# Kernel optimization log

Measured on AMD Instinct MI355X. Metric: run time of the kernel, lower is better.

The kernel has to match this reference:

```python
import jax, jax.numpy as jnp
import numpy as np

IN_DIM, H1, H2, H3, LATENT = 1024, 1024, 512, 256, 256
D, K, BETA = 32, 2048, 0.25
B = 16384


def _leaky(x):
    return jax.nn.leaky_relu(x, negative_slope=0.01)


def setup_inputs() -> dict:
    key = jax.random.key(0)
    ks = jax.random.split(key, 18)
    def lin(k, fan_in, fan_out):
        kw, kb = jax.random.split(k)
        s = 1.0 / np.sqrt(fan_in)
        W = jax.random.uniform(kw, (fan_in, fan_out), jnp.float32, -s, s)
        b = jax.random.uniform(kb, (fan_out,), jnp.float32, -s, s)
        return W, b
    We1, be1 = lin(ks[0], IN_DIM, H1)
    We2, be2 = lin(ks[1], H1, H2)
    We3, be3 = lin(ks[2], H2, H3)
    We4, be4 = lin(ks[3], H3, LATENT)
    Wd1, bd1 = lin(ks[4], LATENT, H3)
    Wd2, bd2 = lin(ks[5], H3, H2)
    Wd3, bd3 = lin(ks[6], H2, H1)
    Wd4, bd4 = lin(ks[7], H1, IN_DIM)
    E = jax.random.uniform(ks[8], (K, D), jnp.float32, -1.0 / K, 1.0 / K)  # codebook
    x = jax.random.uniform(ks[9], (B, IN_DIM), jnp.float32)
    return {"x": x, "We1": We1, "be1": be1, "We2": We2, "be2": be2,
            "We3": We3, "be3": be3, "We4": We4, "be4": be4, "E": E,
            "Wd1": Wd1, "bd1": bd1, "Wd2": Wd2, "bd2": bd2,
            "Wd3": Wd3, "bd3": bd3, "Wd4": Wd4, "bd4": bd4}


def reference(x, We1, be1, We2, be2, We3, be3, We4, be4, E,
              Wd1, bd1, Wd2, bd2, Wd3, bd3, Wd4, bd4):
    # encoder MLP
    h = _leaky(x @ We1 + be1)
    h = _leaky(h @ We2 + be2)
    h = _leaky(h @ We3 + be3)
    z = h @ We4 + be4                      # [B, LATENT]
    # vector quantizer
    zr = z.reshape(-1, D)                  # [N, D], N = B*LATENT/D
    dist = (jnp.sum(zr * zr, axis=1, keepdims=True)
            + jnp.sum(E * E, axis=1)
            - 2.0 * zr @ E.T)              # [N, K]
    idx = jnp.argmin(dist, axis=1)         # [N]
    # one-hot @ E == direct gather of nearest codebook rows
    q = E[idx].reshape(z.shape)            # [B, LATENT]
    commit = jnp.mean(jnp.sum(jnp.square(jax.lax.stop_gradient(q) - z), axis=1))
    embed = jnp.mean(jnp.sum(jnp.square(q - jax.lax.stop_gradient(z)), axis=1))
    vq_loss = BETA * commit + embed
    e = z + jax.lax.stop_gradient(q - z)   # straight-through
    # decoder MLP
    h = _leaky(e @ Wd1 + bd1)
    h = _leaky(h @ Wd2 + bd2)
    h = _leaky(h @ Wd3 + bd3)
    recon = jax.nn.sigmoid(h @ Wd4 + bd4)
    recon_loss = jnp.mean(jnp.sum(jnp.square(recon - x), axis=-1))
    loss = recon_loss + vq_loss
    return z, e, recon, loss, recon_loss, vq_loss
```

## Files before the change

kernel.cpp:

```cpp
#include <hip/hip_runtime.h>
#include <stdint.h>

typedef __attribute__((ext_vector_type(8))) _Float16 half8;
typedef __attribute__((ext_vector_type(4))) _Float16 half4;
typedef __attribute__((ext_vector_type(4))) float f32x4;

__device__ __forceinline__ void gload_lds16(const void* g, void* l) {
  __builtin_amdgcn_global_load_lds(
      (const __attribute__((address_space(1))) void*)g,
      (__attribute__((address_space(3))) void*)l, 16, 0, 0);
}

template <int EPI, int BM, int BN>
__global__ __launch_bounds__(256, ((BM + BN) >= 256 ? 2 : ((BM + BN) == 192 ? 3 : 4)))
void gemm_bt(
    const _Float16* __restrict__ A, const _Float16* __restrict__ Bt,
    const float* __restrict__ bias, _Float16* __restrict__ Ch,
    float* __restrict__ Cf, int M, int N, int Kd,
    const _Float16* __restrict__ Xref, float* __restrict__ lossAcc) {
  constexpr int WM = BM / 2, WN = BN / 2;
  constexpr int MF = WM / 16, NF = WN / 16;
  constexpr int CA = BM / 32, CB = BN / 32;
  constexpr int CHUNKS = CA + CB;
  constexpr int STAGE = (BM + BN) * 64;
  __shared__ __align__(16) _Float16 smem[2 * STAGE];
  float* red = (float*)smem + 64 * BN;

  const int tid = threadIdx.x;
  const int lane = tid & 63;
  const int wav = tid >> 6;
  const int nx = gridDim.x;
  const int nwg = nx * (int)gridDim.y;
  int bid = (int)blockIdx.y * nx + (int)blockIdx.x;
  bid = (bid & 7) * (nwg >> 3) + (bid >> 3);
  const int shift = 31 - __clz(nx);
  const int m0 = (bid >> shift) * BM;
  const int n0 = (bid & (nx - 1)) * BN;
  const int wm = (wav >> 1) * WM;
  const int wn = (wav & 1) * WN;
  const int l15 = lane & 15;
  const int quad = lane >> 4;

  f32x4 acc[MF][NF];
#pragma unroll
  for (int i = 0; i < MF; i++)
#pragma unroll
    for (int j = 0; j < NF; j++) acc[i][j] = (f32x4){0.f, 0.f, 0.f, 0.f};

  auto issue = [&](int kt, int b) {
    _Float16* As = smem + b * STAGE;
    _Float16* Bs = As + BM * 64;
#pragma unroll
    for (int j = 0; j < CA; j++) {
      const int ci = j * 256 + tid;
      const int row = ci >> 3;
      const int kc = ((ci & 7) ^ (row & 7)) << 3;
      gload_lds16(A + (size_t)(m0 + row) * Kd + kt + kc, &As[ci * 8]);
    }
#pragma unroll
    for (int j = 0; j < CB; j++) {
      const int ci = j * 256 + tid;
      const int row = ci >> 3;
      const int kc = ((ci & 7) ^ (row & 7)) << 3;
      gload_lds16(Bt + (size_t)(n0 + row) * Kd + kt + kc, &Bs[ci * 8]);
    }
  };

  int buf = 0;
  issue(0, 0);
  for (int kt = 0; kt < Kd; kt += 64) {
    if (kt + 64 < Kd) {
      issue(kt + 64, buf ^ 1);
      asm volatile("s_waitcnt vmcnt(%0)" ::"i"(CHUNKS) : "memory");
    } else {
      asm volatile("s_waitcnt vmcnt(0)" ::: "memory");
    }
    asm volatile("s_barrier" ::: "memory");

    const _Float16* As = smem + buf * STAGE;
    const _Float16* Bs = As + BM * 64;
#pragma unroll
    for (int s = 0; s < 2; s++) {
      half8 af[MF], bq[NF];
#pragma unroll
      for (int i = 0; i < MF; i++) {
        const int ra = wm + i * 16 + l15;
        const int ca = (s * 4 + quad) ^ (ra & 7);
        af[i] = *(const half8*)&As[ra * 64 + ca * 8];
      }
#pragma unroll
      for (int i = 0; i < NF; i++) {
        const int rb = wn + i * 16 + l15;
        const int cb = (s * 4 + quad) ^ (rb & 7);
        bq[i] = *(const half8*)&Bs[rb * 64 + cb * 8];
      }
#pragma unroll
      for (int mi = 0; mi < MF; mi++)
#pragma unroll
        for (int ni = 0; ni < NF; ni++)
          acc[mi][ni] = __builtin_amdgcn_mfma_f32_16x16x32_f16(af[mi], bq[ni],
                                                               acc[mi][ni], 0, 0, 0);
    }
    asm volatile("s_barrier" ::: "memory");
    buf ^= 1;
  }

  float lsum = 0.f;
  float* eb = (float*)smem;
  constexpr int DIV = BN / 4;
#pragma unroll
  for (int p = 0; p < BM / 64; p++) {
    __syncthreads();
    if ((wm >> 6) == p) {
#pragma unroll
      for (int mi = 0; mi < MF; mi++)
#pragma unroll
        for (int ni = 0; ni < NF; ni++)
#pragma unroll
          for (int r = 0; r < 4; r++) {
            const int rl = (wm & 63) + mi * 16 + quad * 4 + r;
            const int cl = wn + ni * 16 + l15;
            eb[rl * BN + cl] = acc[mi][ni][r];
          }
    }
    __syncthreads();
#pragma unroll
    for (int j = 0; j < BN / 16; j++) {
      const int c = j * 256 + tid;
      const int rl = c / DIV;
      const int cl = (c % DIV) * 4;
      const f32x4 v = *(const f32x4*)&eb[rl * BN + cl];
      const int gcol = n0 + cl;
      const f32x4 bv = *(const f32x4*)&bias[gcol];
      const size_t o = (size_t)(m0 + p * 64 + rl) * N + gcol;
      if (EPI == 0) {
        half4 h;
#pragma unroll
        for (int q = 0; q < 4; q++) {
          float t = v[q] + bv[q];
          t = t > 0.f ? t : 0.01f * t;
          h[q] = (_Float16)t;
        }
        *(half4*)&Ch[o] = h;
      } else if (EPI == 1) {
        f32x4 t;
        half4 h;
#pragma unroll
        for (int q = 0; q < 4; q++) {
          t[q] = v[q] + bv[q];
          h[q] = (_Float16)t[q];
        }
        *(f32x4*)&Cf[o] = t;
        *(half4*)&Ch[o] = h;
      } else {
        const half4 xr = *(const half4*)&Xref[o];
        f32x4 sv;
#pragma unroll
        for (int q = 0; q < 4; q++) {
          const float s = 1.f / (1.f + __expf(-(v[q] + bv[q])));
          sv[q] = s;
          const float d = s - (float)xr[q];
          lsum += d * d;
        }
        *(f32x4*)&Cf[o] = sv;
      }
    }
  }
  if (EPI == 2) {
    __syncthreads();
    red[tid] = lsum;
    __syncthreads();
    for (int s = 128; s > 0; s >>= 1) {
      if (tid < s) red[tid] += red[tid + s];
      __syncthreads();
    }
    if (tid == 0) atomicAdd(lossAcc, red[0]);
  }
}

__global__ __launch_bounds__(256, 4) void vq_argmin(
    const _Float16* __restrict__ zh, const _Float16* __restrict__ Ehf,
    const float* __restrict__ E, const float* __restrict__ ek2,
    float* __restrict__ e_out, _Float16* __restrict__ eh_out,
    float* __restrict__ vq_acc) {
  __shared__ __align__(16) _Float16 Es[512 * 32];
  __shared__ float ek2s[512];
  __shared__ float z2s[128];
  __shared__ int idxs[128];
  __shared__ float vred[256];

  const int tid = threadIdx.x;
  const int lane = tid & 63;
  const int wav = tid >> 6;
  const int l15 = lane & 15;
  const int quad = lane >> 4;
  const int rbase = blockIdx.x * 128 + wav * 32;
  constexpr unsigned KEYMASK = 0xFFFFF800u;

  half8 zf[2];
  float z2p[2];
#pragma unroll
  for (int m = 0; m < 2; m++) {
    zf[m] = *(const half8*)(zh + ((size_t)(rbase + m * 16 + l15)) * 32 + quad * 8);
    float s = 0.f;
#pragma unroll
    for (int j = 0; j < 8; j++) {
      float v = (float)zf[m][j];
      s += v * v;
    }
    s += __shfl_xor(s, 16);
    s += __shfl_xor(s, 32);
    z2p[m] = s;
  }
  if (quad == 0) {
#pragma unroll
    for (int m = 0; m < 2; m++) z2s[wav * 32 + m * 16 + l15] = z2p[m];
  }

  float key[2][4];
#pragma unroll
  for (int m = 0; m < 2; m++)
#pragma unroll
    for (int r = 0; r < 4; r++) key[m][r] = 1e30f;

  for (int cb = 0; cb < 2048; cb += 512) {
    __syncthreads();
#pragma unroll
    for (int j = 0; j < 8; j++) {
      const int u = j * 256 + tid;
      gload_lds16(Ehf + (size_t)cb * 32 + u * 8, &Es[u * 8]);
    }
    if (tid < 128) gload_lds16(&ek2[cb + tid * 4], &ek2s[tid * 4]);
    __syncthreads();

    int idxv = cb + l15;
    for (int c16 = 0; c16 < 32; c16++) {
      const half8 ef = *(const half8*)&Es[(c16 * 64 + lane) * 8];
      const float e2 = ek2s[c16 * 16 + l15];
      const f32x4 cinit = (f32x4){e2, e2, e2, e2};
      f32x4 d0 = __builtin_amdgcn_mfma_f32_16x16x32_f16(zf[0], ef, cinit, 0, 0, 0);
      f32x4 d1 = __builtin_amdgcn_mfma_f32_16x16x32_f16(zf[1], ef, cinit, 0, 0, 0);
#pragma unroll
      for (int r = 0; r < 4; r++) {
        key[0][r] = fminf(key[0][r],
                          __uint_as_float((__float_as_uint(d0[r]) & KEYMASK) | idxv));
        key[1][r] = fminf(key[1][r],
                          __uint_as_float((__float_as_uint(d1[r]) & KEYMASK) | idxv));
      }
      idxv += 16;
    }
  }

#pragma unroll
  for (int off = 1; off < 16; off <<= 1)
#pragma unroll
    for (int m = 0; m < 2; m++)
#pragma unroll
      for (int r = 0; r < 4; r++)
        key[m][r] = fminf(key[m][r], __shfl_xor(key[m][r], off));

  float vpart = 0.f;
  if (l15 == 0) {
#pragma unroll
    for (int m = 0; m < 2; m++)
#pragma unroll
      for (int r = 0; r < 4; r++) {
        const unsigned kb = __float_as_uint(key[m][r]);
        const int rl = wav * 32 + m * 16 + quad * 4 + r;
        idxs[rl] = (int)(kb & 0x7FFu);
        vpart += z2s[rl] + __uint_as_float(kb & KEYMASK);
      }
  }
  vred[tid] = vpart;
  __syncthreads();
  for (int s = 128; s > 0; s >>= 1) {
    if (tid < s) vred[tid] += vred[tid + s];
    __syncthreads();
  }
  if (tid == 0) atomicAdd(vq_acc, vred[0]);

#pragma unroll
  for (int it = 0; it < 2; it++) {
    const int slot = it * 256 + tid;
    const int rowb = slot >> 2, part = slot & 3;
    const int idx = idxs[rowb];
    const size_t orow = ((size_t)blockIdx.x * 128 + rowb) * 32 + part * 8;
    const f32x4 ea = *(const f32x4*)(E + (size_t)idx * 32 + part * 8);
    const f32x4 ebv = *(const f32x4*)(E + (size_t)idx * 32 + part * 8 + 4);
    *(f32x4*)(e_out + orow) = ea;
    *(f32x4*)(e_out + orow + 4) = ebv;
    half8 ehv;
#pragma unroll
    for (int j = 0; j < 4; j++) {
      ehv[j] = (_Float16)ea[j];
      ehv[j + 4] = (_Float16)ebv[j];
    }
    *(half8*)(eh_out + orow) = ehv;
  }
}

struct PrepArgs {
  const float* W[8];
  _Float16* Wt[8];
  int Kw[8], Nw[8];
  int base[9];
  const float* x;
  _Float16* xh;
  const float* E;
  _Float16* Ehf;
  float* ek2;
};

__global__ __launch_bounds__(256) void prep_k(PrepArgs a) {
  __shared__ float t[32][33];
  const int b = blockIdx.x;
  const int tid = threadIdx.x;
  if (b < 8192) {
    const size_t i = (size_t)b * 256 + tid;
    const f32x4 va = *(const f32x4*)(a.x + i * 8);
    const f32x4 vb = *(const f32x4*)(a.x + i * 8 + 4);
    half8 h;
#pragma unroll
    for (int j = 0; j < 4; j++) {
      h[j] = (_Float16)va[j];
      h[j + 4] = (_Float16)vb[j];
    }
    *(half8*)(a.xh + i * 8) = h;
    return;
  }
  if (b < 8192 + 3456) {
    int l = b - 8192;
    int w = 0;
    while (l >= a.base[w + 1]) w++;
    l -= a.base[w];
    const float* W = a.W[w];
    _Float16* Wt = a.Wt[w];
    const int K = a.Kw[w], N = a.Nw[w];
    const int nb = N >> 5;
    const int bx = (l % nb) * 32, by = (l / nb) * 32;
    const int tx = tid & 31, ty = tid >> 5;
#pragma unroll
    for (int i = 0; i < 32; i += 8)
      t[ty + i][tx] = W[(size_t)(by + ty + i) * N + bx + tx];
    __syncthreads();
#pragma unroll
    for (int i = 0; i < 32; i += 8)
      Wt[(size_t)(bx + ty + i) * K + by + tx] = (_Float16)t[tx][ty + i];
    return;
  }
  const int c = (b - 8192 - 3456) * 256 + tid;
  float s = 0.f;
#pragma unroll
  for (int k = 0; k < 32; k++) {
    const float v = a.E[(size_t)c * 32 + k];
    s += v * v;
    a.Ehf[(size_t)((c >> 4) * 64 + (k >> 3) * 16 + (c & 15)) * 8 + (k & 7)] =
        (_Float16)(-2.f * v);
  }
  a.ek2[c] = s;
}

__global__ void finalize_k(const float* __restrict__ scal, float* __restrict__ out) {
  const float vq = 1.25f * (scal[0] / 16384.f);
  const float rl = scal[1] / 16384.f;
  out[0] = rl + vq;
  out[1] = rl;
  out[2] = vq;
}

extern "C" void kernel_launch(void* const* d_in, const int* in_sizes, int n_in,
                              void* d_out, int out_size, void* d_ws, size_t ws_size,
                              hipStream_t stream) {
  const float* x = (const float*)d_in[0];
  const float* be1 = (const float*)d_in[2];
  const float* be2 = (const float*)d_in[4];
  const float* be3 = (const float*)d_in[6];
  const float* be4 = (const float*)d_in[8];
  const float* E = (const float*)d_in[9];
  const float* bd1 = (const float*)d_in[11];
  const float* bd2 = (const float*)d_in[13];
  const float* bd3 = (const float*)d_in[15];
  const float* bd4 = (const float*)d_in[17];

  float* out = (float*)d_out;
  char* ws = (char*)d_ws;

  size_t off = 0;
  auto alloc = [&](size_t bytes) {
    size_t r = off;
    off += (bytes + 255) & ~(size_t)255;
    return r;
  };
  const size_t oXH = alloc((size_t)16384 * 1024 * 2);
  const size_t oWT1 = alloc((size_t)1024 * 1024 * 2);
  const size_t oWT2 = alloc((size_t)512 * 1024 * 2);
  const size_t oWT3 = alloc((size_t)256 * 512 * 2);
  const size_t oWT4 = alloc((size_t)256 * 256 * 2);
  const size_t oWD1 = alloc((size_t)256 * 256 * 2);
  const size_t oWD2 = alloc((size_t)512 * 256 * 2);
  const size_t oWD3 = alloc((size_t)1024 * 512 * 2);
  const size_t oWD4 = alloc((size_t)1024 * 1024 * 2);
  const size_t oEHF = alloc((size_t)2048 * 32 * 2);
  const size_t oEK2 = alloc((size_t)2048 * 4);
  const size_t oSC = alloc(256);
  const size_t oZH = alloc((size_t)16384 * 256 * 2);
  const size_t oQH = alloc((size_t)16384 * 256 * 2);
  const size_t oH1 = alloc((size_t)16384 * 1024 * 2);
  const size_t oH2 = alloc((size_t)16384 * 512 * 2);
  const size_t oH3 = alloc((size_t)16384 * 256 * 2);

  _Float16* xh = (_Float16*)(ws + oXH);
  _Float16* WT1 = (_Float16*)(ws + oWT1);
  _Float16* WT2 = (_Float16*)(ws + oWT2);
  _Float16* WT3 = (_Float16*)(ws + oWT3);
  _Float16* WT4 = (_Float16*)(ws + oWT4);
  _Float16* WD1 = (_Float16*)(ws + oWD1);
  _Float16* WD2 = (_Float16*)(ws + oWD2);
  _Float16* WD3 = (_Float16*)(ws + oWD3);
  _Float16* WD4 = (_Float16*)(ws + oWD4);
  _Float16* Ehf = (_Float16*)(ws + oEHF);
  float* ek2 = (float*)(ws + oEK2);
  float* scal = (float*)(ws + oSC);
  _Float16* zhw = (_Float16*)(ws + oZH);
  _Float16* qh = (_Float16*)(ws + oQH);
  _Float16* h1 = (_Float16*)(ws + oH1);
  _Float16* h2 = (_Float16*)(ws + oH2);
  _Float16* h3 = (_Float16*)(ws + oH3);

  float* zout = out;
  float* eout = out + (size_t)16384 * 256;
  float* rout = out + (size_t)16384 * 256 * 2;
  float* sout = rout + (size_t)16384 * 1024;

  hipMemsetAsync(ws + oSC, 0, 8, stream);

  PrepArgs pa;
  pa.W[0] = (const float*)d_in[1];  pa.Wt[0] = WT1; pa.Kw[0] = 1024; pa.Nw[0] = 1024;
  pa.W[1] = (const float*)d_in[3];  pa.Wt[1] = WT2; pa.Kw[1] = 1024; pa.Nw[1] = 512;
  pa.W[2] = (const float*)d_in[5];  pa.Wt[2] = WT3; pa.Kw[2] = 512;  pa.Nw[2] = 256;
  pa.W[3] = (const float*)d_in[7];  pa.Wt[3] = WT4; pa.Kw[3] = 256;  pa.Nw[3] = 256;
  pa.W[4] = (const float*)d_in[10]; pa.Wt[4] = WD1; pa.Kw[4] = 256;  pa.Nw[4] = 256;
  pa.W[5] = (const float*)d_in[12]; pa.Wt[5] = WD2; pa.Kw[5] = 256;  pa.Nw[5] = 512;
  pa.W[6] = (const float*)d_in[14]; pa.Wt[6] = WD3; pa.Kw[6] = 512;  pa.Nw[6] = 1024;
  pa.W[7] = (const float*)d_in[16]; pa.Wt[7] = WD4; pa.Kw[7] = 1024; pa.Nw[7] = 1024;
  int acc = 0;
  for (int w = 0; w < 8; w++) {
    pa.base[w] = acc;
    acc += (pa.Kw[w] >> 5) * (pa.Nw[w] >> 5);
  }
  pa.base[8] = acc;
  pa.x = x; pa.xh = xh; pa.E = E; pa.Ehf = Ehf; pa.ek2 = ek2;

  dim3 blk(256);
  prep_k<<<8192 + 3456 + 8, blk, 0, stream>>>(pa);

  gemm_bt<0, 128, 128><<<dim3(8, 128), blk, 0, stream>>>(
      xh, WT1, be1, h1, nullptr, 16384, 1024, 1024, nullptr, nullptr);
  gemm_bt<0, 128, 128><<<dim3(4, 128), blk, 0, stream>>>(
      h1, WT2, be2, h2, nullptr, 16384, 512, 1024, nullptr, nullptr);
  gemm_bt<0, 64, 64><<<dim3(4, 256), blk, 0, stream>>>(
      h2, WT3, be3, h3, nullptr, 16384, 256, 512, nullptr, nullptr);
  gemm_bt<1, 64, 64><<<dim3(4, 256), blk, 0, stream>>>(
      h3, WT4, be4, zhw, zout, 16384, 256, 256, nullptr, nullptr);
  vq_argmin<<<1024, blk, 0, stream>>>(zhw, Ehf, E, ek2, eout, qh, &scal[0]);
  gemm_bt<0, 64, 64><<<dim3(4, 256), blk, 0, stream>>>(
      qh, WD1, bd1, h3, nullptr, 16384, 256, 256, nullptr, nullptr);
  gemm_bt<0, 128, 128><<<dim3(4, 128), blk, 0, stream>>>(
      h3, WD2, bd2, h2, nullptr, 16384, 512, 256, nullptr, nullptr);
  gemm_bt<0, 128, 128><<<dim3(8, 128), blk, 0, stream>>>(
      h2, WD3, bd3, h1, nullptr, 16384, 1024, 512, nullptr, nullptr);
  gemm_bt<2, 128, 128><<<dim3(8, 128), blk, 0, stream>>>(
      h1, WD4, bd4, nullptr, rout, 16384, 1024, 1024, xh, &scal[1]);
  finalize_k<<<1, 1, 0, stream>>>(scal, sout);
}
```

Before: 397.7 us.

## Add 256x256-tile 8-wave pipelined GEMM for the three largest layers

Adds a new GEMM kernel with 256x256 output tiles, 8 waves and 128KB of dynamic LDS. It double-buffers K tiles, splits each tile into four sub-blocks whose loads are interleaved with MFMA phases, and raises wave priority around the MFMAs. It also remaps workgroup IDs in an XCD-aware order. The kernel replaces the 128x128 kernel for the encoder's first layer and the last two decoder layers, aiming for more data reuse per load and better overlap of loads with MFMA work. The cost is fewer, larger workgroups (256 per launch) and heavy LDS and register use, which may limit occupancy and wave balance across CUs.

```diff
diff --git a/kernel.cpp b/kernel.cpp
--- a/kernel.cpp
+++ b/kernel.cpp
@@ -9,6 +9,211 @@
   __builtin_amdgcn_global_load_lds(
       (const __attribute__((address_space(1))) void*)g,
       (__attribute__((address_space(3))) void*)l, 16, 0, 0);
+}
+
+#define GBAR asm volatile("s_barrier" ::: "memory")
+#define LGKM0                                            \
+  asm volatile("s_waitcnt lgkmcnt(0)" ::: "memory");     \
+  __builtin_amdgcn_sched_barrier(0)
+
+#define MMA_Q(QM, QN)                                                        \
+  __builtin_amdgcn_s_setprio(1);                                             \
+  _Pragma("unroll") for (int s = 0; s < 2; s++)                              \
+  _Pragma("unroll") for (int i = 0; i < 4; i++)                              \
+  _Pragma("unroll") for (int j = 0; j < 2; j++)                              \
+      acc[(QM) * 4 + i][(QN) * 2 + j] = __builtin_amdgcn_mfma_f32_16x16x32_f16( \
+          af[i][s], bq[j][s], acc[(QM) * 4 + i][(QN) * 2 + j], 0, 0, 0);     \
+  __builtin_amdgcn_s_setprio(0);
+
+template <int EPI>
+__global__ __launch_bounds__(512, 2) void gemm8p(
+    const _Float16* __restrict__ A, const _Float16* __restrict__ Bt,
+    const float* __restrict__ bias, _Float16* __restrict__ Ch,
+    float* __restrict__ Cf, int M, int N, int Kd,
+    const _Float16* __restrict__ Xref, float* __restrict__ lossAcc) {
+  extern __shared__ __align__(16) char dyn[];
+
+  const int tid = threadIdx.x;
+  const int lane = tid & 63;
+  const int wav = tid >> 6;
+  const int wr = wav >> 2;
+  const int wc = wav & 3;
+  const int l15 = lane & 15;
+  const int quad = lane >> 4;
+
+  const int nx = gridDim.x;
+  const int nwg = nx * (int)gridDim.y;
+  int bid = (int)blockIdx.y * nx + (int)blockIdx.x;
+  bid = (bid & 7) * (nwg >> 3) + (bid >> 3);
+  const int shift = 31 - __clz(nx);
+  const int m0 = (bid >> shift) * 256;
+  const int n0 = (bid & (nx - 1)) * 256;
+
+  f32x4 acc[8][4];
+#pragma unroll
+  for (int i = 0; i < 8; i++)
+#pragma unroll
+    for (int j = 0; j < 4; j++) acc[i][j] = (f32x4){0.f, 0.f, 0.f, 0.f};
+
+  auto stageA = [&](int kt, int slot, int RB) {
+    const int row = RB + (tid >> 3);
+    const int ch = tid & 7;
+    const int gm = m0 + ((row >> 6) & 1) * 128 + (row >> 7) * 64 + (row & 63);
+    const int kc = (ch ^ (row & 7)) << 3;
+    gload_lds16(A + (size_t)gm * Kd + kt + kc,
+                dyn + slot * 65536 + row * 128 + ch * 16);
+  };
+  auto stageB = [&](int kt, int slot, int RB) {
+    const int row = RB + (tid >> 3);
+    const int ch = tid & 7;
+    const int gn = n0 + ((row >> 5) & 3) * 64 + (row >> 7) * 32 + (row & 31);
+    const int kc = (ch ^ (row & 7)) << 3;
+    gload_lds16(Bt + (size_t)gn * Kd + kt + kc,
+                dyn + slot * 65536 + 32768 + row * 128 + ch * 16);
+  };
+
+  half8 af[4][2], bq[2][2];
+  auto dsA = [&](const _Float16* As, int qm) {
+#pragma unroll
+    for (int i = 0; i < 4; i++) {
+      const int ra = qm * 128 + wr * 64 + i * 16 + l15;
+#pragma unroll
+      for (int s = 0; s < 2; s++)
+        af[i][s] = *(const half8*)&As[ra * 64 + (((s * 4 + quad) ^ (ra & 7)) << 3)];
+    }
+  };
+  auto dsB = [&](const _Float16* Bs, int qn) {
+#pragma unroll
+    for (int j = 0; j < 2; j++) {
+      const int rb = qn * 128 + wc * 32 + j * 16 + l15;
+#pragma unroll
+      for (int s = 0; s < 2; s++)
+        bq[j][s] = *(const half8*)&Bs[rb * 64 + (((s * 4 + quad) ^ (rb & 7)) << 3)];
+    }
+  };
+
+  const int NT = Kd >> 6;
+
+  stageA(0, 0, 0);
+  stageA(0, 0, 64);
+  stageB(0, 0, 128);
+  stageB(0, 0, 192);
+  stageA(0, 0, 128);
+  stageA(0, 0, 192);
+  stageB(0, 0, 0);
+  stageB(0, 0, 64);
+  stageA(64, 1, 0);
+  stageA(64, 1, 64);
+  stageB(64, 1, 128);
+  stageB(64, 1, 192);
+  asm volatile("s_waitcnt vmcnt(4)" ::: "memory");
+  GBAR;
+
+  for (int t = 0; t < NT; ++t) {
+    const int slot = t & 1;
+    const int nsl = slot ^ 1;
+    const int kt1 = (t + 1) << 6;
+    const int kt2 = (t + 2) << 6;
+    const bool p1 = (t + 1) < NT;
+    const bool p2 = (t + 2) < NT;
+    const _Float16* As = (const _Float16*)(dyn + slot * 65536);
+    const _Float16* Bs = (const _Float16*)(dyn + slot * 65536 + 32768);
+
+    dsA(As, 0);
+    dsB(Bs, 0);
+    if (p1) { stageA(kt1, nsl, 128); stageA(kt1, nsl, 192); }
+    GBAR;
+    LGKM0;
+    MMA_Q(0, 0);
+    GBAR;
+    dsB(Bs, 1);
+    if (p1) { stageB(kt1, nsl, 0); stageB(kt1, nsl, 64); }
+    GBAR;
+    LGKM0;
+    MMA_Q(0, 1);
+    GBAR;
+    dsA(As, 1);
+    if (p2) { stageA(kt2, slot, 0); stageA(kt2, slot, 64); }
+    GBAR;
+    LGKM0;
+    MMA_Q(1, 1);
+    GBAR;
+    dsB(Bs, 0);
+    if (p2) { stageB(kt2, slot, 128); stageB(kt2, slot, 192); }
+    GBAR;
+    LGKM0;
+    MMA_Q(1, 0);
+    if (p2) {
+      asm volatile("s_waitcnt vmcnt(4)" ::: "memory");
+    } else {
+      asm volatile("s_waitcnt vmcnt(0)" ::: "memory");
+    }
+    GBAR;
+  }
+
+  float lsum = 0.f;
+  float* eb = (float*)dyn;
+  float* red = (float*)dyn + 64 * 256;
+#pragma unroll
+  for (int p = 0; p < 4; p++) {
+    __syncthreads();
+    if (wr == (p >> 1)) {
+#pragma unroll
+      for (int mi2 = 0; mi2 < 4; mi2++) {
+        const int mi = (p & 1) * 4 + mi2;
+#pragma unroll
+        for (int ni = 0; ni < 4; ni++)
+#pragma unroll
+          for (int r = 0; r < 4; r++) {
+            const int rl = mi2 * 16 + quad * 4 + r;
+            const int cl = wc * 64 + ni * 16 + l15;
+            eb[rl * 256 + cl] = acc[mi][ni][r];
+          }
+      }
+    }
+    __syncthreads();
+#pragma unroll
+    for (int j = 0; j < 8; j++) {
+      const int c = j * 512 + tid;
+      const int rl = c >> 6;
+      const int cl = (c & 63) * 4;
+      const f32x4 v = *(const f32x4*)&eb[rl * 256 + cl];
+      const int gcol = n0 + cl;
+      const f32x4 bv = *(const f32x4*)&bias[gcol];
+      const size_t o = (size_t)(m0 + p * 64 + rl) * N + gcol;
+      if (EPI == 0) {
+        half4 h;
+#pragma unroll
+        for (int q = 0; q < 4; q++) {
+          float tv = v[q] + bv[q];
+          tv = tv > 0.f ? tv : 0.01f * tv;
+          h[q] = (_Float16)tv;
+        }
+        *(half4*)&Ch[o] = h;
+      } else {
+        const half4 xr = *(const half4*)&Xref[o];
+        f32x4 sv;
+#pragma unroll
+        for (int q = 0; q < 4; q++) {
+          const float sg = 1.f / (1.f + __expf(-(v[q] + bv[q])));
+          sv[q] = sg;
+          const float d = sg - (float)xr[q];
+          lsum += d * d;
+        }
+        *(f32x4*)&Cf[o] = sv;
+      }
+    }
+  }
+  if (EPI == 2) {
+    __syncthreads();
+    red[tid] = lsum;
+    __syncthreads();
+    for (int s = 256; s > 0; s >>= 1) {
+      if (tid < s) red[tid] += red[tid + s];
+      __syncthreads();
+    }
+    if (tid == 0) atomicAdd(lossAcc, red[0]);
+  }
 }
 
 template <int EPI, int BM, int BN>
@@ -81,7 +286,7 @@
     const _Float16* Bs = As + BM * 64;
 #pragma unroll
     for (int s = 0; s < 2; s++) {
-      half8 af[MF], bq[NF];
+      half8 af[MF], bqv[NF];
 #pragma unroll
       for (int i = 0; i < MF; i++) {
         const int ra = wm + i * 16 + l15;
@@ -92,13 +297,13 @@
       for (int i = 0; i < NF; i++) {
         const int rb = wn + i * 16 + l15;
         const int cb = (s * 4 + quad) ^ (rb & 7);
-        bq[i] = *(const half8*)&Bs[rb * 64 + cb * 8];
+        bqv[i] = *(const half8*)&Bs[rb * 64 + cb * 8];
       }
 #pragma unroll
       for (int mi = 0; mi < MF; mi++)
 #pragma unroll
         for (int ni = 0; ni < NF; ni++)
-          acc[mi][ni] = __builtin_amdgcn_mfma_f32_16x16x32_f16(af[mi], bq[ni],
+          acc[mi][ni] = __builtin_amdgcn_mfma_f32_16x16x32_f16(af[mi], bqv[ni],
                                                                acc[mi][ni], 0, 0, 0);
     }
     asm volatile("s_barrier" ::: "memory");
@@ -434,6 +639,11 @@
 
   hipMemsetAsync(ws + oSC, 0, 8, stream);
 
+  hipFuncSetAttribute((const void*)gemm8p<0>,
+                      hipFuncAttributeMaxDynamicSharedMemorySize, 131072);
+  hipFuncSetAttribute((const void*)gemm8p<2>,
+                      hipFuncAttributeMaxDynamicSharedMemorySize, 131072);
+
   PrepArgs pa;
   pa.W[0] = (const float*)d_in[1];  pa.Wt[0] = WT1; pa.Kw[0] = 1024; pa.Nw[0] = 1024;
   pa.W[1] = (const float*)d_in[3];  pa.Wt[1] = WT2; pa.Kw[1] = 1024; pa.Nw[1] = 512;
@@ -454,7 +664,7 @@
   dim3 blk(256);
   prep_k<<<8192 + 3456 + 8, blk, 0, stream>>>(pa);
 
-  gemm_bt<0, 128, 128><<<dim3(8, 128), blk, 0, stream>>>(
+  gemm8p<0><<<dim3(4, 64), dim3(512), 131072, stream>>>(
       xh, WT1, be1, h1, nullptr, 16384, 1024, 1024, nullptr, nullptr);
   gemm_bt<0, 128, 128><<<dim3(4, 128), blk, 0, stream>>>(
       h1, WT2, be2, h2, nullptr, 16384, 512, 1024, nullptr, nullptr);
@@ -467,9 +677,9 @@
       qh, WD1, bd1, h3, nullptr, 16384, 256, 256, nullptr, nullptr);
   gemm_bt<0, 128, 128><<<dim3(4, 128), blk, 0, stream>>>(
       h3, WD2, bd2, h2, nullptr, 16384, 512, 256, nullptr, nullptr);
-  gemm_bt<0, 128, 128><<<dim3(8, 128), blk, 0, stream>>>(
+  gemm8p<0><<<dim3(4, 64), dim3(512), 131072, stream>>>(
       h2, WD3, bd3, h1, nullptr, 16384, 1024, 512, nullptr, nullptr);
-  gemm_bt<2, 128, 128><<<dim3(8, 128), blk, 0, stream>>>(
+  gemm8p<2><<<dim3(4, 64), dim3(512), 131072, stream>>>(
       h1, WD4, bd4, nullptr, rout, 16384, 1024, 1024, xh, &scal[1]);
   finalize_k<<<1, 1, 0, stream>>>(scal, sout);
 }
```

New measurement: 381.7 us. 1.04x faster.
